# Performance work log

Hardware: AMD Instinct MI355X
Metric: run time of the kernel (lower is better)

The kernel has to match this reference:

```python
import jax, jax.numpy as jnp
import numpy as np

N = 50000
E = 800000
NODE_IN, EDGE_IN, HID, OUT, L = 32, 16, 128, 128, 2


def _layer_norm(h, g, b, eps=1e-5):
    mu = jnp.mean(h, axis=-1, keepdims=True)
    var = jnp.var(h, axis=-1, keepdims=True)
    return (h - mu) * jax.lax.rsqrt(var + eps) * g + b


def setup_inputs() -> dict:
    key = jax.random.key(0)
    ks = jax.random.split(key, 20)
    s = lambda k, shape, fan: jax.random.normal(k, shape, jnp.float32) * (1.0 / np.sqrt(fan))
    return {
        "x": jax.random.normal(ks[0], (N, NODE_IN), jnp.float32),
        "edge_index": jax.random.randint(ks[1], (2, E), 0, N, jnp.int64),
        "edge_attr": jax.random.normal(ks[2], (E, EDGE_IN), jnp.float32),
        "enc_W": s(ks[3], (NODE_IN, HID), NODE_IN),
        "enc_b": jnp.zeros((HID,), jnp.float32),
        "enc_g": jnp.ones((HID,), jnp.float32),
        "enc_beta": jnp.zeros((HID,), jnp.float32),
        "msg_W1": s(ks[4], (L, 2 * HID + EDGE_IN, HID), 2 * HID + EDGE_IN),
        "msg_b1": jnp.zeros((L, HID), jnp.float32),
        "msg_W2": s(ks[5], (L, HID, HID), HID),
        "msg_b2": jnp.zeros((L, HID), jnp.float32),
        "upd_W1": s(ks[6], (L, 2 * HID, HID), 2 * HID),
        "upd_b1": jnp.zeros((L, HID), jnp.float32),
        "upd_W2": s(ks[7], (L, HID, HID), HID),
        "upd_b2": jnp.zeros((L, HID), jnp.float32),
        "ln_g": jnp.ones((L, HID), jnp.float32),
        "ln_beta": jnp.zeros((L, HID), jnp.float32),
        "head_W": s(ks[8], (HID, OUT), HID),
        "head_b": jnp.zeros((OUT,), jnp.float32),
    }


def reference(x, edge_index, edge_attr, enc_W, enc_b, enc_g, enc_beta,
              msg_W1, msg_b1, msg_W2, msg_b2, upd_W1, upd_b1, upd_W2, upd_b2,
              ln_g, ln_beta, head_W, head_b):
    src = edge_index[0]  # x_j (source)
    tgt = edge_index[1]  # x_i (target, aggregation index)
    n = x.shape[0]

    # node encoder: Linear -> ReLU -> LayerNorm
    h = jax.nn.relu(x @ enc_W + enc_b)
    h = _layer_norm(h, enc_g, enc_beta)

    # per-edge incoming-degree for mean aggregation (isolated nodes -> 0)
    cnt = jax.ops.segment_sum(jnp.ones((tgt.shape[0],), h.dtype), tgt, num_segments=n)
    denom = jnp.maximum(cnt, 1.0)[:, None]

    for l in range(L):
        x_i = h[tgt]                                 # [E, HID]
        x_j = h[src]                                 # [E, HID]
        msg_in = jnp.concatenate([x_i, x_j, edge_attr], axis=-1)  # [E, 2H+Ed]
        m = jax.nn.relu(msg_in @ msg_W1[l] + msg_b1[l]) @ msg_W2[l] + msg_b2[l]
        aggr = jax.ops.segment_sum(m, tgt, num_segments=n) / denom  # mean
        upd_in = jnp.concatenate([h, aggr], axis=-1)
        out = jax.nn.relu(upd_in @ upd_W1[l] + upd_b1[l]) @ upd_W2[l] + upd_b2[l]
        h = _layer_norm(h + out, ln_g[l], ln_beta[l])

    return h @ head_W + head_b
```

## Files before the change

### kernel.cpp

```cpp
#include <hip/hip_runtime.h>
#include <hip/hip_bf16.h>
#include <stdint.h>

#define N_NODES 50000
#define N_EDGES 800000
#define NL 2

#define KS2 136
#define KSU 264
#define ESTR 133

typedef __bf16 bf16x8 __attribute__((ext_vector_type(8)));
typedef float f32x4 __attribute__((ext_vector_type(4)));

__device__ __forceinline__ f32x4 mfma_bf16(uint4 a, uint4 b, f32x4 c) {
    return __builtin_amdgcn_mfma_f32_16x16x32_bf16(
        __builtin_bit_cast(bf16x8, a), __builtin_bit_cast(bf16x8, b), c, 0, 0, 0);
}

__device__ __forceinline__ unsigned short f2b(float f) {
    union { float f; unsigned u; } v; v.f = f;
    unsigned r = v.u + 0x7FFFu + ((v.u >> 16) & 1u);
    return (unsigned short)(r >> 16);
}

__device__ __forceinline__ float b2f(unsigned short u) {
    union { unsigned u; float f; } v; v.u = ((unsigned)u) << 16; return v.f;
}
__device__ __forceinline__ float b2f_lo(unsigned u) {
    union { unsigned u; float f; } v; v.u = u << 16; return v.f;
}
__device__ __forceinline__ float b2f_hi(unsigned u) {
    union { unsigned u; float f; } v; v.u = u & 0xFFFF0000u; return v.f;
}

template<int KSTEPS, int BSTR>
__device__ __forceinline__ void gemm8(const unsigned short* aLane,
                                      const unsigned short* bLane, f32x4 acc[8]) {
#pragma unroll
    for (int kc = 0; kc < KSTEPS; kc++) {
        uint4 a = *(const uint4*)(aLane + kc * 32);
#pragma unroll
        for (int ct = 0; ct < 8; ct++) {
            uint4 b = *(const uint4*)(bLane + (size_t)ct * 16 * BSTR + kc * 32);
            acc[ct] = mfma_bf16(a, b, acc[ct]);
        }
    }
}

template<int KSTEPS, int ASTR, int BSTR>
__device__ __forceinline__ void gemm_2x4(const unsigned short* aLane,
                                         const unsigned short* bLane,
                                         f32x4 acc[4][2]) {
#pragma unroll
    for (int kc = 0; kc < KSTEPS; kc++) {
        uint4 b0 = *(const uint4*)(bLane + kc * 32);
        uint4 b1 = *(const uint4*)(bLane + (size_t)16 * BSTR + kc * 32);
#pragma unroll
        for (int rt = 0; rt < 4; rt++) {
            uint4 a = *(const uint4*)(aLane + (size_t)rt * 16 * ASTR + kc * 32);
            acc[rt][0] = mfma_bf16(a, b0, acc[rt][0]);
            acc[rt][1] = mfma_bf16(a, b1, acc[rt][1]);
        }
    }
}

__global__ void prep_kernel(const float* __restrict__ mW1,
                            const float* __restrict__ uW1, const float* __restrict__ uW2,
                            const float* __restrict__ hW,
                            unsigned short* __restrict__ wab, unsigned short* __restrict__ w1cp,
                            unsigned short* __restrict__ u1t, unsigned short* __restrict__ u2t,
                            unsigned short* __restrict__ ht) {
    int i = blockIdx.x * 256 + threadIdx.x;
    const int SA = NL * 256 * 136;
    const int SC = NL * 128 * 32;
    const int SU = NL * 128 * KSU;
    const int S3 = NL * 128 * KS2;
    const int S4 = 128 * KS2;
    if (i < SA) {
        int l = i / (256 * 136), r = i % (256 * 136), j = r / 136, k = r % 136;
        float v = 0.f;
        if (k < 128)
            v = (j < 128) ? mW1[((size_t)l * 272 + k) * 128 + j]
                          : mW1[((size_t)l * 272 + 128 + k) * 128 + (j - 128)];
        wab[i] = f2b(v);
        return;
    }
    i -= SA;
    if (i < SC) {
        int l = i / (128 * 32), r = i % (128 * 32), j = r / 32, k = r % 32;
        w1cp[i] = (k < 16) ? f2b(mW1[((size_t)l * 272 + 256 + k) * 128 + j]) : (unsigned short)0;
        return;
    }
    i -= SC;
    if (i < SU) {
        int l = i / (128 * KSU), r = i % (128 * KSU), n = r / KSU, k = r % KSU;
        if (k < 128)       u1t[i] = f2b(uW1[((size_t)l * 256 + k) * 128 + n]);
        else if (k >= 256) u1t[i] = 0;
        return;
    }
    i -= SU;
    if (i < S3) {
        int l = i / (128 * KS2), r = i % (128 * KS2), n = r / KS2, k = r % KS2;
        u2t[i] = (k < 128) ? f2b(uW2[((size_t)l * 128 + k) * 128 + n]) : (unsigned short)0;
        return;
    }
    i -= S3;
    if (i < S4) {
        int n = i / KS2, k = i % KS2;
        ht[i] = (k < 128) ? f2b(hW[(size_t)k * 128 + n]) : (unsigned short)0;
    }
}

__global__ void prep2_kernel(const float* __restrict__ mW2, const float* __restrict__ uW1,
                             unsigned short* __restrict__ u1t) {
    __shared__ float w2row[128];
    const int l = blockIdx.x >> 7, j = blockIdx.x & 127;
    const int n = threadIdx.x;
    w2row[n] = mW2[((size_t)l * 128 + j) * 128 + n];
    __syncthreads();
    float s = 0.f;
#pragma unroll 8
    for (int c = 0; c < 128; c++)
        s += w2row[c] * uW1[((size_t)l * 256 + 128 + c) * 128 + n];
    u1t[(size_t)l * 128 * KSU + (size_t)n * KSU + 128 + j] = f2b(s);
}

__global__ void prep3_kernel(const float* __restrict__ mb2, const float* __restrict__ uW1,
                             float* __restrict__ bfold) {
    const int l = blockIdx.x;
    const int n = threadIdx.x;
    float s = 0.f;
#pragma unroll 8
    for (int c = 0; c < 128; c++)
        s += mb2[l * 128 + c] * uW1[((size_t)l * 256 + 128 + c) * 128 + n];
    bfold[l * 128 + n] = s;
}

__global__ __launch_bounds__(256) void enc_kernel(
        const float* __restrict__ x, const float* __restrict__ W,
        const float* __restrict__ b, const float* __restrict__ g, const float* __restrict__ bet,
        float* __restrict__ h, unsigned short* __restrict__ hb) {
    __shared__ float sx[64];
    __shared__ float redS[4], redSS[4];
    const int t = threadIdx.x;
    const int nb = blockIdx.x * 2;
    if (t < 64) sx[t] = x[(size_t)nb * 32 + t];
    __syncthreads();
    const int half = t >> 7, j = t & 127;
    const int node = nb + half;
    float acc = b[j];
#pragma unroll
    for (int k = 0; k < 32; k++) acc += sx[half * 32 + k] * W[k * 128 + j];
    float v = fmaxf(acc, 0.f);
    float s = v, ss = v * v;
#pragma unroll
    for (int d = 32; d > 0; d >>= 1) { s += __shfl_down(s, d); ss += __shfl_down(ss, d); }
    const int wv = t >> 6;
    if ((t & 63) == 0) { redS[wv] = s; redSS[wv] = ss; }
    __syncthreads();
    float S = redS[half * 2] + redS[half * 2 + 1];
    float SS = redSS[half * 2] + redSS[half * 2 + 1];
    float mu = S * (1.f / 128.f);
    float var = SS * (1.f / 128.f) - mu * mu;
    float rs = rsqrtf(var + 1e-5f);
    float o = (v - mu) * rs * g[j] + bet[j];
    h[(size_t)node * 128 + j] = o;
    hb[(size_t)node * 128 + j] = f2b(o);
}

__global__ void hist_kernel(const int* __restrict__ tgt, int* __restrict__ hist) {
    int i = blockIdx.x * 256 + threadIdx.x;
    atomicAdd(hist + tgt[i], 1);
}

__global__ void scan1_kernel(const int* __restrict__ hist, int* __restrict__ incl,
                             int* __restrict__ blksum) {
    __shared__ int buf[256];
    const int t = threadIdx.x;
    const int i = blockIdx.x * 256 + t;
    int v = (i < N_NODES) ? hist[i] : 0;
    buf[t] = v; __syncthreads();
#pragma unroll
    for (int d = 1; d < 256; d <<= 1) {
        int x = (t >= d) ? buf[t - d] : 0;
        __syncthreads();
        buf[t] += x;
        __syncthreads();
    }
    if (i < N_NODES) incl[i] = buf[t];
    if (t == 255) blksum[blockIdx.x] = buf[255];
}

__global__ void scan2_kernel(int* __restrict__ blksum, int nblk) {
    __shared__ int buf[256];
    const int t = threadIdx.x;
    int v = (t < nblk) ? blksum[t] : 0;
    buf[t] = v; __syncthreads();
#pragma unroll
    for (int d = 1; d < 256; d <<= 1) {
        int x = (t >= d) ? buf[t - d] : 0;
        __syncthreads();
        buf[t] += x;
        __syncthreads();
    }
    if (t < nblk) blksum[t] = buf[t];
}

__global__ void scan3_kernel(int* __restrict__ incl, const int* __restrict__ blksum,
                             const int* __restrict__ hist) {
    const int i = blockIdx.x * 256 + threadIdx.x;
    if (i >= N_NODES) return;
    const int b = blockIdx.x;
    const int base = (b > 0) ? blksum[b - 1] : 0;
    incl[i] = incl[i] + base - hist[i];
}

__global__ void scatter_kernel(const int* __restrict__ src, const int* __restrict__ tgt,
                               const float* __restrict__ ea, int* __restrict__ cursor,
                               unsigned short* __restrict__ sSrc, unsigned short* __restrict__ sTgt,
                               unsigned short* __restrict__ eabS) {
    const int e = blockIdx.x * 256 + threadIdx.x;
    const int tg = tgt[e];
    const int p = atomicAdd(cursor + tg, 1);
    sSrc[p] = (unsigned short)src[e];
    sTgt[p] = (unsigned short)tg;
    const float4* s = (const float4*)(ea + (size_t)e * 16);
    ushort4* d = (ushort4*)(eabS + (size_t)p * 16);
#pragma unroll
    for (int i = 0; i < 4; i++) {
        float4 v = s[i];
        d[i] = make_ushort4(f2b(v.x), f2b(v.y), f2b(v.z), f2b(v.w));
    }
}

__global__ __launch_bounds__(256, 4) void node_kernel(
        const unsigned short* __restrict__ hb, const unsigned short* __restrict__ wab,
        const float* __restrict__ b1,
        unsigned short* __restrict__ Tb, unsigned short* __restrict__ Sb) {
    __shared__ __align__(16) unsigned short As[64 * KS2];
    const int t = threadIdx.x;
    const int n0 = blockIdx.x * 64;
    {
        const int m = t >> 2, q = t & 3;
        const int node = n0 + m;
        uint4* dst = (uint4*)(As + m * KS2);
        if (node < N_NODES) {
            const uint4* s = (const uint4*)(hb + (size_t)node * 128);
#pragma unroll
            for (int i = 0; i < 4; i++) dst[q * 4 + i] = s[q * 4 + i];
        } else {
            uint4 z{0, 0, 0, 0};
            for (int i = q; i < 16; i += 4) dst[i] = z;
        }
    }
    __syncthreads();

    const int wv = t >> 6, lane = t & 63, lr = lane & 15, lq = lane >> 4;
    const int cb = wv * 64;
    const f32x4 z4 = {0.f, 0.f, 0.f, 0.f};
    f32x4 acc[4][4];
#pragma unroll
    for (int i = 0; i < 4; i++)
#pragma unroll
        for (int j = 0; j < 4; j++) acc[i][j] = z4;

    const unsigned short* aL = As + lr * KS2 + lq * 8;
    const unsigned short* bL = wab + (size_t)(cb + lr) * KS2 + lq * 8;
#pragma unroll
    for (int kc = 0; kc < 4; kc++) {
        uint4 bA = *(const uint4*)(bL + kc * 32);
        uint4 bB = *(const uint4*)(bL + (size_t)16 * KS2 + kc * 32);
        uint4 bC = *(const uint4*)(bL + (size_t)32 * KS2 + kc * 32);
        uint4 bD = *(const uint4*)(bL + (size_t)48 * KS2 + kc * 32);
#pragma unroll
        for (int rt = 0; rt < 4; rt++) {
            uint4 a = *(const uint4*)(aL + (size_t)rt * 16 * KS2 + kc * 32);
            acc[rt][0] = mfma_bf16(a, bA, acc[rt][0]);
            acc[rt][1] = mfma_bf16(a, bB, acc[rt][1]);
            acc[rt][2] = mfma_bf16(a, bC, acc[rt][2]);
            acc[rt][3] = mfma_bf16(a, bD, acc[rt][3]);
        }
    }
#pragma unroll
    for (int ct = 0; ct < 4; ct++) {
        const int j = cb + ct * 16 + lr;
        const float bias = (j < 128) ? b1[j] : 0.f;
#pragma unroll
        for (int rt = 0; rt < 4; rt++) {
#pragma unroll
            for (int r = 0; r < 4; r++) {
                const int node = n0 + rt * 16 + lq * 4 + r;
                if (node < N_NODES) {
                    const float v = acc[rt][ct][r] + bias;
                    if (j < 128) Tb[(size_t)node * 128 + j] = f2b(v);
                    else         Sb[(size_t)node * 128 + (j - 128)] = f2b(v);
                }
            }
        }
    }
}

__global__ __launch_bounds__(256, 4) void edge_kernel(
        const unsigned short* __restrict__ eabS,
        const unsigned short* __restrict__ sSrc, const unsigned short* __restrict__ sTgt,
        const unsigned short* __restrict__ w1cp,
        const unsigned short* __restrict__ Tb, const unsigned short* __restrict__ Sb,
        float* __restrict__ aggr) {
    __shared__ float Es[64 * ESTR];
    __shared__ int sT[64];
    __shared__ int sS[64];

    const int t = threadIdx.x;
    const int e0 = blockIdx.x * 64;
    if (t < 64) { sT[t] = sTgt[e0 + t]; sS[t] = sSrc[e0 + t]; }

    const int wv = t >> 6, lane = t & 63, lr = lane & 15, lq = lane >> 4;
    const f32x4 z4 = {0.f, 0.f, 0.f, 0.f};
    {
        uint4 a = {0, 0, 0, 0};
        if (lq < 2) a = *(const uint4*)(eabS + (size_t)(e0 + wv * 16 + lr) * 16 + lq * 8);
        f32x4 acc[8];
#pragma unroll
        for (int ct = 0; ct < 8; ct++) {
            uint4 b = *(const uint4*)(w1cp + (ct * 16 + lr) * 32 + lq * 8);
            acc[ct] = mfma_bf16(a, b, z4);
        }
#pragma unroll
        for (int ct = 0; ct < 8; ct++) {
            const int col = ct * 16 + lr;
#pragma unroll
            for (int r = 0; r < 4; r++)
                Es[(wv * 16 + lq * 4 + r) * ESTR + col] = acc[ct][r];
        }
    }
    __syncthreads();

    {
        const int m = t & 63;
        const int c8b = t >> 6;
        const unsigned short* Trow = Tb + (size_t)sT[m] * 128;
        const unsigned short* Srow = Sb + (size_t)sS[m] * 128;
        float* Erow = Es + m * ESTR;
#pragma unroll
        for (int it = 0; it < 4; it++) {
            const int c0 = (c8b + it * 4) * 8;
            const uint4 tv = *(const uint4*)(Trow + c0);
            const uint4 sv = *(const uint4*)(Srow + c0);
            float tf[8] = {b2f_lo(tv.x), b2f_hi(tv.x), b2f_lo(tv.y), b2f_hi(tv.y),
                           b2f_lo(tv.z), b2f_hi(tv.z), b2f_lo(tv.w), b2f_hi(tv.w)};
            float sf[8] = {b2f_lo(sv.x), b2f_hi(sv.x), b2f_lo(sv.y), b2f_hi(sv.y),
                           b2f_lo(sv.z), b2f_hi(sv.z), b2f_lo(sv.w), b2f_hi(sv.w)};
#pragma unroll
            for (int i = 0; i < 8; i++)
                Erow[c0 + i] = fmaxf(Erow[c0 + i] + tf[i] + sf[i], 0.f);
        }
    }
    __syncthreads();

    {
        const int c = t >> 1;
        const int rb = (t & 1) * 32;
        float s = 0.f;
        int cur = sT[rb];
        for (int i = 0; i < 32; i++) {
            const int rg = rb + i;
            const int tg = sT[rg];
            if (tg != cur) {
                atomicAdd(aggr + (size_t)cur * 128 + c, s);
                s = 0.f; cur = tg;
            }
            s += Es[rg * ESTR + c];
        }
        atomicAdd(aggr + (size_t)cur * 128 + c, s);
    }
}

__global__ __launch_bounds__(256, 4) void upd_kernel(
        const unsigned short* __restrict__ hb_in, const float* __restrict__ h_in,
        const float* __restrict__ aggr, const int* __restrict__ hist,
        const unsigned short* __restrict__ u1t, const unsigned short* __restrict__ u2t,
        const float* __restrict__ b1, const float* __restrict__ bf,
        const float* __restrict__ b2,
        const float* __restrict__ g, const float* __restrict__ bet,
        float* __restrict__ h_out, unsigned short* __restrict__ hb_out) {
    __shared__ __align__(16) char smemA[64 * KSU * 2];
    __shared__ float sF[64];
    unsigned short* As = (unsigned short*)smemA;
    float* LNb = (float*)smemA;

    const int t = threadIdx.x;
    const int n0 = blockIdx.x * 64;
    {
        const int m = t >> 2, q = t & 3;
        const int node = n0 + m;
        unsigned short* row = As + m * KSU;
        if (node < N_NODES) {
            const uint4* ph = (const uint4*)(hb_in + (size_t)node * 128);
            uint4* d0 = (uint4*)row;
#pragma unroll
            for (int i = 0; i < 4; i++) d0[q * 4 + i] = ph[q * 4 + i];
            const int cntv = hist[node];
            if (q == 0) sF[m] = (cntv > 0) ? 1.f : 0.f;
            const float rden = 1.0f / fmaxf((float)cntv, 1.0f);
            const float4* pa = (const float4*)(aggr + (size_t)node * 128 + q * 32);
            ushort4* d1 = (ushort4*)(row + 128 + q * 32);
#pragma unroll
            for (int i = 0; i < 8; i++) {
                float4 v = pa[i];
                d1[i] = make_ushort4(f2b(v.x * rden), f2b(v.y * rden),
                                     f2b(v.z * rden), f2b(v.w * rden));
            }
            if (q == 0) { uint4 z{0, 0, 0, 0}; ((uint4*)(row + 256))[0] = z; }
        } else {
            if (q == 0) sF[m] = 0.f;
            uint4 z{0, 0, 0, 0};
            uint4* d = (uint4*)row;
            for (int i = q; i < 33; i += 4) d[i] = z;
        }
    }
    __syncthreads();

    const int wv = t >> 6, lane = t & 63, lr = lane & 15, lq = lane >> 4;
    const int cb = wv * 32;
    const f32x4 z4 = {0.f, 0.f, 0.f, 0.f};

    f32x4 acc[4][2];
#pragma unroll
    for (int i = 0; i < 4; i++) { acc[i][0] = z4; acc[i][1] = z4; }
    gemm_2x4<8, KSU, KSU>(As + lr * KSU + lq * 8,
                          u1t + (size_t)(cb + lr) * KSU + lq * 8, acc);
    __syncthreads();

#pragma unroll
    for (int ct = 0; ct < 2; ct++) {
        const int col = cb + ct * 16 + lr;
        const float bv = b1[col];
        const float bfv = bf[col];
#pragma unroll
        for (int rt = 0; rt < 4; rt++) {
#pragma unroll
            for (int r = 0; r < 4; r++) {
                const int ml = rt * 16 + lq * 4 + r;
                float v = fmaxf(acc[rt][ct][r] + bv + sF[ml] * bfv, 0.f);
                As[ml * KSU + col] = f2b(v);
            }
        }
    }
    __syncthreads();

    f32x4 acc2[4][2];
#pragma unroll
    for (int i = 0; i < 4; i++) { acc2[i][0] = z4; acc2[i][1] = z4; }
    gemm_2x4<4, KSU, KS2>(As + lr * KSU + lq * 8,
                          u2t + (size_t)(cb + lr) * KS2 + lq * 8, acc2);
    __syncthreads();

#pragma unroll
    for (int ct = 0; ct < 2; ct++) {
        const int col = cb + ct * 16 + lr;
        const float bv = b2[col];
#pragma unroll
        for (int rt = 0; rt < 4; rt++) {
#pragma unroll
            for (int r = 0; r < 4; r++) {
                const int ml = rt * 16 + lq * 4 + r;
                const int node = n0 + ml;
                if (node < N_NODES)
                    LNb[ml * 132 + col] = acc2[rt][ct][r] + bv + h_in[(size_t)node * 128 + col];
            }
        }
    }
    __syncthreads();

    {
        const int r = t >> 2, c0 = (t & 3) * 32;
        const int node = n0 + r;
        if (node < N_NODES) {
            float s = 0.f, ss = 0.f;
#pragma unroll
            for (int i = 0; i < 32; i++) { float v = LNb[r * 132 + c0 + i]; s += v; ss += v * v; }
            s += __shfl_xor(s, 1); ss += __shfl_xor(ss, 1);
            s += __shfl_xor(s, 2); ss += __shfl_xor(ss, 2);
            const float mu = s * (1.0f / 128.0f);
            const float var = ss * (1.0f / 128.0f) - mu * mu;
            const float rs = rsqrtf(var + 1e-5f);
#pragma unroll
            for (int i = 0; i < 32; i++) {
                const int j = c0 + i;
                float v = (LNb[r * 132 + j] - mu) * rs * g[j] + bet[j];
                h_out[(size_t)node * 128 + j] = v;
                hb_out[(size_t)node * 128 + j] = f2b(v);
            }
        }
    }
}

__global__ __launch_bounds__(256, 2) void head_kernel(
        const unsigned short* __restrict__ hb, const unsigned short* __restrict__ ht,
        const float* __restrict__ hbias, float* __restrict__ out) {
    __shared__ __align__(16) unsigned short As[64 * KS2];
    const int t = threadIdx.x;
    const int n0 = blockIdx.x * 64;
    {
        const int m = t >> 2, q = t & 3;
        const int node = n0 + m;
        uint4* dst = (uint4*)(As + m * KS2);
        if (node < N_NODES) {
            const uint4* s = (const uint4*)(hb + (size_t)node * 128);
#pragma unroll
            for (int i = 0; i < 4; i++) dst[q * 4 + i] = s[q * 4 + i];
        } else {
            uint4 z{0, 0, 0, 0};
            for (int i = q; i < 16; i += 4) dst[i] = z;
        }
    }
    __syncthreads();

    const int wv = t >> 6, lane = t & 63, lr = lane & 15, lq = lane >> 4;
    const int m0 = wv * 16;
    const f32x4 z4 = {0.f, 0.f, 0.f, 0.f};
    f32x4 acc[8];
#pragma unroll
    for (int i = 0; i < 8; i++) acc[i] = z4;
    gemm8<4, KS2>(As + (m0 + lr) * KS2 + lq * 8, ht + (size_t)lr * KS2 + lq * 8, acc);
#pragma unroll
    for (int ct = 0; ct < 8; ct++) {
        const int col = ct * 16 + lr;
        const float bv = hbias[col];
#pragma unroll
        for (int r = 0; r < 4; r++) {
            const int node = n0 + m0 + lq * 4 + r;
            if (node < N_NODES) out[(size_t)node * 128 + col] = acc[ct][r] + bv;
        }
    }
}

extern "C" void kernel_launch(void* const* d_in, const int* in_sizes, int n_in,
                              void* d_out, int out_size, void* d_ws, size_t ws_size,
                              hipStream_t stream) {
    const float* x       = (const float*)d_in[0];
    const int*   ei      = (const int*)d_in[1];
    const float* ea      = (const float*)d_in[2];
    const float* encW    = (const float*)d_in[3];
    const float* encb    = (const float*)d_in[4];
    const float* encg    = (const float*)d_in[5];
    const float* encbeta = (const float*)d_in[6];
    const float* msgW1   = (const float*)d_in[7];
    const float* msgb1   = (const float*)d_in[8];
    const float* msgW2   = (const float*)d_in[9];
    const float* msgb2   = (const float*)d_in[10];
    const float* updW1   = (const float*)d_in[11];
    const float* updb1   = (const float*)d_in[12];
    const float* updW2   = (const float*)d_in[13];
    const float* updb2   = (const float*)d_in[14];
    const float* lng     = (const float*)d_in[15];
    const float* lnbeta  = (const float*)d_in[16];
    const float* headW   = (const float*)d_in[17];
    const float* headb   = (const float*)d_in[18];

    char* w = (char*)d_ws;
    size_t off = 0;
    auto nxt = [&](size_t bytes) -> void* {
        void* p = w + off;
        off = (off + bytes + 255) & ~(size_t)255;
        return p;
    };
    float*          h     = (float*)nxt((size_t)N_NODES * 128 * 4);
    unsigned short* hb    = (unsigned short*)nxt((size_t)N_NODES * 128 * 2);
    float*          aggr  = (float*)nxt((size_t)N_NODES * 128 * 4);
    unsigned short* Tb    = (unsigned short*)nxt((size_t)N_NODES * 128 * 2);
    unsigned short* Sb    = (unsigned short*)nxt((size_t)N_NODES * 128 * 2);
    unsigned short* eabS  = (unsigned short*)nxt((size_t)N_EDGES * 16 * 2);
    unsigned short* sSrc  = (unsigned short*)nxt((size_t)N_EDGES * 2);
    unsigned short* sTgtS = (unsigned short*)nxt((size_t)N_EDGES * 2);
    int*            hist  = (int*)nxt((size_t)N_NODES * 4);
    int*            incl  = (int*)nxt((size_t)N_NODES * 4);
    int*            blksum= (int*)nxt(256 * 4);
    unsigned short* wab   = (unsigned short*)nxt((size_t)NL * 256 * 136 * 2);
    unsigned short* w1cp  = (unsigned short*)nxt((size_t)NL * 128 * 32 * 2);
    unsigned short* u1t   = (unsigned short*)nxt((size_t)NL * 128 * KSU * 2);
    unsigned short* u2t   = (unsigned short*)nxt((size_t)NL * 128 * KS2 * 2);
    unsigned short* ht    = (unsigned short*)nxt((size_t)128 * KS2 * 2);
    float*          bfold = (float*)nxt((size_t)NL * 128 * 4);

    const int NBLK = (N_NODES + 255) / 256;
    const int PREP_N = NL * 256 * 136 + NL * 128 * 32 + NL * 128 * KSU
                     + NL * 128 * KS2 + 128 * KS2;

    hipMemsetAsync(hist, 0, (size_t)N_NODES * 4, stream);
    prep_kernel<<<(PREP_N + 255) / 256, 256, 0, stream>>>(msgW1, updW1, updW2, headW,
                                                          wab, w1cp, u1t, u2t, ht);
    prep2_kernel<<<NL * 128, 128, 0, stream>>>(msgW2, updW1, u1t);
    prep3_kernel<<<NL, 128, 0, stream>>>(msgb2, updW1, bfold);
    enc_kernel<<<25000, 256, 0, stream>>>(x, encW, encb, encg, encbeta, h, hb);
    hist_kernel<<<3125, 256, 0, stream>>>(ei + N_EDGES, hist);
    scan1_kernel<<<NBLK, 256, 0, stream>>>(hist, incl, blksum);
    scan2_kernel<<<1, 256, 0, stream>>>(blksum, NBLK);
    scan3_kernel<<<NBLK, 256, 0, stream>>>(incl, blksum, hist);
    scatter_kernel<<<3125, 256, 0, stream>>>(ei, ei + N_EDGES, ea, incl,
                                             sSrc, sTgtS, eabS);

    for (int l = 0; l < NL; l++) {
        node_kernel<<<782, 256, 0, stream>>>(hb, wab + (size_t)l * 256 * 136,
                                             msgb1 + l * 128, Tb, Sb);
        hipMemsetAsync(aggr, 0, (size_t)N_NODES * 128 * 4, stream);
        edge_kernel<<<12500, 256, 0, stream>>>(eabS, sSrc, sTgtS,
                                               w1cp + (size_t)l * 128 * 32,
                                               Tb, Sb, aggr);
        upd_kernel<<<782, 256, 0, stream>>>(hb, h, aggr, hist,
                                            u1t + (size_t)l * 128 * KSU,
                                            u2t + (size_t)l * 128 * KS2,
                                            updb1 + l * 128, bfold + l * 128,
                                            updb2 + l * 128,
                                            lng + l * 128, lnbeta + l * 128, h, hb);
    }
    head_kernel<<<782, 256, 0, stream>>>(hb, ht, headb, (float*)d_out);
}
```

Measured before the change: 575.5 us.

## Halve edge kernel shared-memory tile to process edges in two halves for occupancy

The edge kernel now stages 32 edges at a time in LDS instead of 64, looping twice per block, and raises the launch-bounds occupancy hint from 4 to 8 blocks per CU. Each wave computes a 16x64 slice of the edge-attribute projection instead of 16x128. The smaller LDS footprint is meant to allow more resident blocks and hide the latency of the random gathers. In exchange there are extra barriers, and only half the threads run each segmented-reduction pass.

```diff
diff --git a/kernel.cpp b/kernel.cpp
--- a/kernel.cpp
+++ b/kernel.cpp
@@ -301,13 +301,13 @@
     }
 }
 
-__global__ __launch_bounds__(256, 4) void edge_kernel(
+__global__ __launch_bounds__(256, 8) void edge_kernel(
         const unsigned short* __restrict__ eabS,
         const unsigned short* __restrict__ sSrc, const unsigned short* __restrict__ sTgt,
         const unsigned short* __restrict__ w1cp,
         const unsigned short* __restrict__ Tb, const unsigned short* __restrict__ Sb,
         float* __restrict__ aggr) {
-    __shared__ float Es[64 * ESTR];
+    __shared__ __align__(16) float Es[32 * ESTR];
     __shared__ int sT[64];
     __shared__ int sS[64];
 
@@ -316,63 +316,71 @@
     if (t < 64) { sT[t] = sTgt[e0 + t]; sS[t] = sSrc[e0 + t]; }
 
     const int wv = t >> 6, lane = t & 63, lr = lane & 15, lq = lane >> 4;
+    const int rtw = (wv >> 1) * 16;
+    const int cbw = (wv & 1) * 64;
     const f32x4 z4 = {0.f, 0.f, 0.f, 0.f};
-    {
-        uint4 a = {0, 0, 0, 0};
-        if (lq < 2) a = *(const uint4*)(eabS + (size_t)(e0 + wv * 16 + lr) * 16 + lq * 8);
-        f32x4 acc[8];
-#pragma unroll
-        for (int ct = 0; ct < 8; ct++) {
-            uint4 b = *(const uint4*)(w1cp + (ct * 16 + lr) * 32 + lq * 8);
-            acc[ct] = mfma_bf16(a, b, z4);
-        }
-#pragma unroll
-        for (int ct = 0; ct < 8; ct++) {
-            const int col = ct * 16 + lr;
-#pragma unroll
-            for (int r = 0; r < 4; r++)
-                Es[(wv * 16 + lq * 4 + r) * ESTR + col] = acc[ct][r];
-        }
-    }
-    __syncthreads();
-
-    {
-        const int m = t & 63;
-        const int c8b = t >> 6;
-        const unsigned short* Trow = Tb + (size_t)sT[m] * 128;
-        const unsigned short* Srow = Sb + (size_t)sS[m] * 128;
-        float* Erow = Es + m * ESTR;
-#pragma unroll
-        for (int it = 0; it < 4; it++) {
-            const int c0 = (c8b + it * 4) * 8;
-            const uint4 tv = *(const uint4*)(Trow + c0);
-            const uint4 sv = *(const uint4*)(Srow + c0);
-            float tf[8] = {b2f_lo(tv.x), b2f_hi(tv.x), b2f_lo(tv.y), b2f_hi(tv.y),
-                           b2f_lo(tv.z), b2f_hi(tv.z), b2f_lo(tv.w), b2f_hi(tv.w)};
-            float sf[8] = {b2f_lo(sv.x), b2f_hi(sv.x), b2f_lo(sv.y), b2f_hi(sv.y),
-                           b2f_lo(sv.z), b2f_hi(sv.z), b2f_lo(sv.w), b2f_hi(sv.w)};
-#pragma unroll
-            for (int i = 0; i < 8; i++)
-                Erow[c0 + i] = fmaxf(Erow[c0 + i] + tf[i] + sf[i], 0.f);
-        }
-    }
-    __syncthreads();
-
-    {
-        const int c = t >> 1;
-        const int rb = (t & 1) * 32;
-        float s = 0.f;
-        int cur = sT[rb];
-        for (int i = 0; i < 32; i++) {
-            const int rg = rb + i;
-            const int tg = sT[rg];
-            if (tg != cur) {
-                atomicAdd(aggr + (size_t)cur * 128 + c, s);
-                s = 0.f; cur = tg;
-            }
-            s += Es[rg * ESTR + c];
-        }
-        atomicAdd(aggr + (size_t)cur * 128 + c, s);
+
+#pragma unroll
+    for (int h = 0; h < 2; h++) {
+        if (h) __syncthreads();
+
+        {
+            uint4 a = {0, 0, 0, 0};
+            if (lq < 2)
+                a = *(const uint4*)(eabS + (size_t)(e0 + h * 32 + rtw + lr) * 16 + lq * 8);
+            f32x4 acc[4];
+#pragma unroll
+            for (int ct = 0; ct < 4; ct++) {
+                uint4 b = *(const uint4*)(w1cp + (cbw + ct * 16 + lr) * 32 + lq * 8);
+                acc[ct] = mfma_bf16(a, b, z4);
+            }
+#pragma unroll
+            for (int ct = 0; ct < 4; ct++) {
+                const int col = cbw + ct * 16 + lr;
+#pragma unroll
+                for (int r = 0; r < 4; r++)
+                    Es[(rtw + lq * 4 + r) * ESTR + col] = acc[ct][r];
+            }
+        }
+        __syncthreads();
+
+        {
+            const int m = t & 31;
+            const int c8b = t >> 5;
+            const int ge = h * 32 + m;
+            const unsigned short* Trow = Tb + (size_t)sT[ge] * 128;
+            const unsigned short* Srow = Sb + (size_t)sS[ge] * 128;
+            float* Erow = Es + m * ESTR;
+#pragma unroll
+            for (int it = 0; it < 2; it++) {
+                const int c0 = (c8b + it * 8) * 8;
+                const uint4 tv = *(const uint4*)(Trow + c0);
+                const uint4 sv = *(const uint4*)(Srow + c0);
+                float tf[8] = {b2f_lo(tv.x), b2f_hi(tv.x), b2f_lo(tv.y), b2f_hi(tv.y),
+                               b2f_lo(tv.z), b2f_hi(tv.z), b2f_lo(tv.w), b2f_hi(tv.w)};
+                float sf[8] = {b2f_lo(sv.x), b2f_hi(sv.x), b2f_lo(sv.y), b2f_hi(sv.y),
+                               b2f_lo(sv.z), b2f_hi(sv.z), b2f_lo(sv.w), b2f_hi(sv.w)};
+#pragma unroll
+                for (int i = 0; i < 8; i++)
+                    Erow[c0 + i] = fmaxf(Erow[c0 + i] + tf[i] + sf[i], 0.f);
+            }
+        }
+        __syncthreads();
+
+        if ((t & 1) == h) {
+            const int c = t >> 1;
+            float s = 0.f;
+            int cur = sT[h * 32];
+            for (int i = 0; i < 32; i++) {
+                const int tg = sT[h * 32 + i];
+                if (tg != cur) {
+                    atomicAdd(aggr + (size_t)cur * 128 + c, s);
+                    s = 0.f; cur = tg;
+                }
+                s += Es[i * ESTR + c];
+            }
+            atomicAdd(aggr + (size_t)cur * 128 + c, s);
+        }
     }
 }
 
```

New measurement: 572.4 us. Within noise of the previous version (-0.5%).
